# Performance work log

Measured on AMD Instinct MI355X. Metric: run time of the kernel, lower is better.

## Reference

```python
import jax, jax.numpy as jnp
import numpy as np

DIM = 384
H_RES, W_RES = 56, 56
HEADS = 12
WS = 7          # window size
SS = 3          # shift size
N = WS * WS     # tokens per window
NW = (H_RES // WS) * (W_RES // WS)
EPS = 1e-5


def _rel_pos_index(ws):
    coords = np.stack(np.meshgrid(np.arange(ws), np.arange(ws), indexing='ij'))  # [2,ws,ws]
    cf = coords.reshape(2, -1)                      # [2, N]
    rc = (cf[:, :, None] - cf[:, None, :]).transpose(1, 2, 0)  # [N,N,2]
    rc[..., 0] += ws - 1
    rc[..., 1] += ws - 1
    rc[..., 0] *= 2 * ws - 1
    return rc.sum(-1)                               # [N,N] int


def _attn_mask(h, w, ws, ss):
    img = np.zeros((h, w))
    cnt = 0
    slices = (slice(0, -ws), slice(-ws, -ss), slice(-ss, None))
    for hs in slices:
        for wsl in slices:
            img[hs, wsl] = cnt
            cnt += 1
    mw = img.reshape(h // ws, ws, w // ws, ws).transpose(0, 2, 1, 3).reshape(-1, ws * ws)  # [nW,N]
    d = mw[:, None, :] - mw[:, :, None]
    return np.where(d != 0, -100.0, 0.0).astype(np.float32)  # [nW,N,N]


RPI = jnp.asarray(_rel_pos_index(WS).reshape(-1))          # [N*N]
ATTN_MASK = jnp.asarray(_attn_mask(H_RES, W_RES, WS, SS))  # [nW,N,N]


def _layernorm(x, g, b):
    mu = jnp.mean(x, axis=-1, keepdims=True)
    var = jnp.mean(jnp.square(x - mu), axis=-1, keepdims=True)
    return (x - mu) * jax.lax.rsqrt(var + EPS) * g + b


def setup_inputs() -> dict:
    key = jax.random.key(0)
    ks = jax.random.split(key, 8)
    s = 0.02
    return {
        'x': jax.random.normal(ks[0], (32, 1 + H_RES * W_RES, DIM), jnp.float32),
        'norm1_g': jnp.ones((DIM,), jnp.float32),
        'norm1_b': jnp.zeros((DIM,), jnp.float32),
        'qkv_w': jax.random.normal(ks[1], (DIM, 3 * DIM), jnp.float32) * s,
        'qkv_b': jnp.zeros((3 * DIM,), jnp.float32),
        'rpb_table': jax.random.normal(ks[2], ((2 * WS - 1) ** 2, HEADS), jnp.float32) * s,
        'proj_w': jax.random.normal(ks[3], (DIM, DIM), jnp.float32) * s,
        'proj_b': jnp.zeros((DIM,), jnp.float32),
        'norm2_g': jnp.ones((DIM,), jnp.float32),
        'norm2_b': jnp.zeros((DIM,), jnp.float32),
        'fc1_w': jax.random.normal(ks[4], (DIM, 4 * DIM), jnp.float32) * s,
        'fc1_b': jnp.zeros((4 * DIM,), jnp.float32),
        'fc2_w': jax.random.normal(ks[5], (4 * DIM, DIM), jnp.float32) * s,
        'fc2_b': jnp.zeros((DIM,), jnp.float32),
    }


def reference(x, norm1_g, norm1_b, qkv_w, qkv_b, rpb_table, proj_w, proj_b,
              norm2_g, norm2_b, fc1_w, fc1_b, fc2_w, fc2_b):
    B = x.shape[0]
    C = DIM
    hd = C // HEADS
    scale = hd ** -0.5

    time_token = x[:, :1, :]          # [B,1,C]
    img = x[:, 1:, :]                 # [B,H*W,C]
    shortcut = img

    h = _layernorm(img, norm1_g, norm1_b).reshape(B, H_RES, W_RES, C)
    h = jnp.roll(h, shift=(-SS, -SS), axis=(1, 2))  # cyclic shift

    # window partition -> [B*nW, N, C]
    xw = h.reshape(B, H_RES // WS, WS, W_RES // WS, WS, C)
    xw = xw.transpose(0, 1, 3, 2, 4, 5).reshape(-1, N, C)

    # window attention
    qkv = (xw @ qkv_w + qkv_b).reshape(-1, N, 3, HEADS, hd).transpose(2, 0, 3, 1, 4)
    q, k, v = qkv[0], qkv[1], qkv[2]                 # [B*nW, H, N, hd]
    attn = jnp.einsum('whnd,whmd->whnm', q * scale, k)
    bias = rpb_table[RPI].reshape(N, N, HEADS).transpose(2, 0, 1)  # [H,N,N]
    attn = attn + bias[None]
    attn = attn.reshape(B, NW, HEADS, N, N) + ATTN_MASK[None, :, None]
    attn = jax.nn.softmax(attn.reshape(-1, HEADS, N, N), axis=-1)
    out = jnp.einsum('whnm,whmd->wnhd', attn, v).reshape(-1, N, C)
    out = out @ proj_w + proj_b

    # window reverse -> [B,H,W,C]
    out = out.reshape(B, H_RES // WS, W_RES // WS, WS, WS, C)
    out = out.transpose(0, 1, 3, 2, 4, 5).reshape(B, H_RES, W_RES, C)
    out = jnp.roll(out, shift=(SS, SS), axis=(1, 2)).reshape(B, H_RES * W_RES, C)

    img = shortcut + out
    x = jnp.concatenate([time_token, img], axis=1)   # [B,1+H*W,C]
    x = _layernorm(x, norm2_g, norm2_b)
    hmlp = jax.nn.gelu(x @ fc1_w + fc1_b, approximate=False)
    x = x + (hmlp @ fc2_w + fc2_b)
    return x
```

## Files before the change

### kernel.cpp

```cpp
#include <hip/hip_runtime.h>
#include <hip/hip_bf16.h>

#define DIM 384
#define HEADS 12
#define NTOK 49
#define TOKENS 3137
#define M_ATTN 100352
#define M_FULL 100384
#define M_PAD  100480
#define SCALEQ 0.17677669529663687f

typedef __attribute__((ext_vector_type(8))) short s8v;
typedef __attribute__((ext_vector_type(4))) float f4v;
typedef unsigned short u16;

__device__ __forceinline__ float b2f(int s) {
  union { unsigned u; float f; } c; c.u = ((unsigned)(s & 0xffff)) << 16; return c.f;
}
__device__ __forceinline__ u16 f2b(float f) {
  __hip_bfloat16 h = __float2bfloat16(f);
  return *reinterpret_cast<u16*>(&h);
}
__device__ __forceinline__ void gload16(const void* g, void* l) {
  __builtin_amdgcn_global_load_lds((const __attribute__((address_space(1))) void*)g,
                                   (__attribute__((address_space(3))) void*)l, 16, 0, 0);
}

__global__ void k_convert(const float* __restrict__ qkv_w, const float* __restrict__ qkv_b,
                          const float* __restrict__ proj_w, const float* __restrict__ fc1_w,
                          const float* __restrict__ fc2_w,
                          u16* __restrict__ wt_qkv, float* __restrict__ qkvb_s,
                          u16* __restrict__ wt_proj, u16* __restrict__ wt_fc1,
                          u16* __restrict__ wt_fc2) {
  int i = blockIdx.x * 256 + threadIdx.x;
  if (i < 1152 * 384) { int n = i / 384, k = i % 384;
    float v = qkv_w[(size_t)k * 1152 + n]; if (n < 384) v *= SCALEQ; wt_qkv[i] = f2b(v); }
  if (i < 1152) qkvb_s[i] = qkv_b[i] * (i < 384 ? SCALEQ : 1.0f);
  if (i < 384 * 384) { int n = i / 384, k = i % 384; wt_proj[i] = f2b(proj_w[(size_t)k * 384 + n]); }
  if (i < 1536 * 384) { int n = i / 384, k = i % 384; wt_fc1[i] = f2b(fc1_w[(size_t)k * 1536 + n]); }
  if (i < 384 * 1536) { int n = i / 1536, k = i % 1536; wt_fc2[i] = f2b(fc2_w[(size_t)k * 384 + n]); }
}

__global__ void k_addtab(const float* __restrict__ rpb, float* __restrict__ ADD) {
  int idx = blockIdx.x * 256 + threadIdx.x;
  if (idx >= 4 * HEADS * NTOK * NTOK) return;
  int j = idx % NTOK, t = idx / NTOK;
  int i = t % NTOK; t /= NTOK;
  int h = t % HEADS; int cls = t / HEADS;
  int ii = i / 7, jj = i % 7, ji = j / 7, j2 = j % 7;
  int rpi = (ii - ji + 6) * 13 + (jj - j2 + 6);
  float v = rpb[rpi * HEADS + h];
  int rh = (cls & 2) ? (ii < 4 ? 1 : 2) : 0;
  int rw = (cls & 1) ? (jj < 4 ? 1 : 2) : 0;
  int sh = (cls & 2) ? (ji < 4 ? 1 : 2) : 0;
  int sw = (cls & 1) ? (j2 < 4 ? 1 : 2) : 0;
  if (rh != sh || rw != sw) v -= 100.0f;
  ADD[idx] = v;
}

__global__ void k_ln1(const float* __restrict__ x, const float* __restrict__ g,
                      const float* __restrict__ b, u16* __restrict__ xw, int t0) {
  int wid = threadIdx.x >> 6, lane = threadIdx.x & 63;
  int t = t0 + blockIdx.x * 4 + wid;
  int bi = t / 3136, rem = t % 3136;
  int win = rem / NTOK, n = rem % NTOK;
  int wh = win >> 3, ww = win & 7, ii = n / 7, jj = n % 7;
  int h = (wh * 7 + ii + 3) % 56;
  int w = (ww * 7 + jj + 3) % 56;
  const float* src = x + ((size_t)bi * TOKENS + 1 + h * 56 + w) * DIM;
  float v[6];
  #pragma unroll
  for (int e = 0; e < 6; e++) v[e] = src[lane + e * 64];
  float s = v[0] + v[1] + v[2] + v[3] + v[4] + v[5];
  #pragma unroll
  for (int m = 1; m < 64; m <<= 1) s += __shfl_xor(s, m);
  float mu = s * (1.0f / 384.0f);
  float q = 0.f;
  #pragma unroll
  for (int e = 0; e < 6; e++) { float d = v[e] - mu; q += d * d; }
  #pragma unroll
  for (int m = 1; m < 64; m <<= 1) q += __shfl_xor(q, m);
  float rstd = rsqrtf(q * (1.0f / 384.0f) + 1e-5f);
  u16* dst = xw + (size_t)(t - t0) * DIM;
  #pragma unroll
  for (int e = 0; e < 6; e++) {
    int c = lane + e * 64;
    dst[c] = f2b((v[e] - mu) * rstd * g[c] + b[c]);
  }
}

template<int MODE>
__global__ __launch_bounds__(256) void k_gemm(
    const u16* __restrict__ A, const u16* __restrict__ Bt,
    const float* __restrict__ bias, u16* __restrict__ Cb,
    float* __restrict__ outp, const u16* __restrict__ resid,
    int N, int K, int row_off) {
  __shared__ __align__(16) u16 As[2][128 * 64];
  __shared__ __align__(16) u16 Bs[2][128 * 64];
  int gx = gridDim.x;
  int lid = blockIdx.y * gx + blockIdx.x;
  int nwg = gx * gridDim.y;
  int q = nwg >> 3, r = nwg & 7;
  int xcd = lid & 7, loc = lid >> 3;
  int tile = (xcd < r ? xcd * (q + 1) : r * (q + 1) + (xcd - r) * q) + loc;
  int m0 = (tile / gx) * 128, n0 = (tile % gx) * 128;
  int t = threadIdx.x;
  int lane = t & 63, wave = t >> 6;
  int lo = lane & 15, hi = lane >> 4;
  int wr = (wave >> 1) * 64, wc = (wave & 1) * 64;
  int rl = lane >> 3;
  int sl = (lane & 7) ^ rl;
  const u16* Ag = A + (size_t)(m0 + wave * 32 + rl) * K + sl * 8;
  const u16* Bg = Bt + (size_t)(n0 + wave * 32 + rl) * K + sl * 8;
  f4v acc[4][4];
  #pragma unroll
  for (int m = 0; m < 4; m++)
    #pragma unroll
    for (int n = 0; n < 4; n++) acc[m][n] = (f4v)(0.0f);
  int nt = K >> 6;
#define STAGE(buf, kt) do {                                              \
    u16* al_ = As[buf] + wave * 32 * 64;                                 \
    u16* bl_ = Bs[buf] + wave * 32 * 64;                                 \
    _Pragma("unroll")                                                    \
    for (int g_ = 0; g_ < 4; g_++) {                                     \
      gload16(Ag + (size_t)(g_ * 8) * K + (kt), al_ + g_ * 8 * 64);      \
      gload16(Bg + (size_t)(g_ * 8) * K + (kt), bl_ + g_ * 8 * 64);      \
    } } while (0)
  STAGE(0, 0);
  for (int kt = 0; kt < nt; ++kt) {
    int c = kt & 1;
    if (kt + 1 < nt) {
      STAGE(1 - c, (kt + 1) << 6);
      asm volatile("s_waitcnt vmcnt(8)" ::: "memory");
    } else {
      asm volatile("s_waitcnt vmcnt(0)" ::: "memory");
    }
    __builtin_amdgcn_s_barrier();
    __builtin_amdgcn_sched_barrier(0);
    s8v af[2][4], bfr[2][4];
    #pragma unroll
    for (int kk = 0; kk < 2; kk++) {
      #pragma unroll
      for (int m = 0; m < 4; m++) {
        int row = wr + m * 16 + lo;
        af[kk][m] = *(const s8v*)(As[c] + row * 64 + (((kk * 4 + hi) ^ (row & 7)) * 8));
      }
      #pragma unroll
      for (int n = 0; n < 4; n++) {
        int row = wc + n * 16 + lo;
        bfr[kk][n] = *(const s8v*)(Bs[c] + row * 64 + (((kk * 4 + hi) ^ (row & 7)) * 8));
      }
    }
    asm volatile("s_waitcnt lgkmcnt(0)" ::: "memory");
    __builtin_amdgcn_sched_barrier(0);
    __builtin_amdgcn_s_barrier();
    __builtin_amdgcn_sched_barrier(0);
    __builtin_amdgcn_s_setprio(1);
    #pragma unroll
    for (int kk = 0; kk < 2; kk++)
      #pragma unroll
      for (int m = 0; m < 4; m++)
        #pragma unroll
        for (int n = 0; n < 4; n++)
          acc[m][n] = __builtin_amdgcn_mfma_f32_16x16x32_bf16(af[kk][m], bfr[kk][n], acc[m][n], 0, 0, 0);
    __builtin_amdgcn_s_setprio(0);
  }
#undef STAGE
  #pragma unroll
  for (int m = 0; m < 4; m++) {
    int grow = m0 + wr + m * 16 + hi * 4;
    #pragma unroll
    for (int n = 0; n < 4; n++) {
      int gcol = n0 + wc + n * 16 + lo;
      float bv = bias[gcol];
      #pragma unroll
      for (int r2 = 0; r2 < 4; r2++) {
        float val = acc[m][n][r2] + bv;
        size_t idx = (size_t)(grow + r2) * N + gcol;
        if (MODE == 0) {
          Cb[idx] = f2b(val);
        } else if (MODE == 1) {
          float u = __builtin_fmaf(0.0713548163f * val, val * val, 1.5957691216f * val);
          float gl = val * __builtin_amdgcn_rcpf(1.0f + __expf(-u));
          Cb[idx] = f2b(gl);
        } else {
          int orow = grow + r2 + row_off;
          if (orow < M_FULL) {
            size_t oi = (size_t)orow * DIM + gcol;
            outp[oi] = val + b2f(resid[oi]);
          }
        }
      }
    }
  }
}

__global__ __launch_bounds__(256) void k_attn2(const u16* __restrict__ qkv,
                                               const float* __restrict__ ADD,
                                               u16* __restrict__ ao, int win0) {
  __shared__ u16 PT[4][64][76];
  __shared__ u16 VT[4][32][76];
  int wid = threadIdx.x >> 6, lane = threadIdx.x & 63;
  int lo = lane & 15, hi = lane >> 4;
  int win_l = blockIdx.x * 4 + wid;
  int nw = (win0 + win_l) & 63;
  int wh = nw >> 3, ww = nw & 7;
  int cls = ((wh == 7) ? 2 : 0) + ((ww == 7) ? 1 : 0);
  size_t rowbase = (size_t)win_l * NTOK;
  u16 (*pt)[76] = PT[wid];
  u16 (*vt)[76] = VT[wid];

  int rcl[4];
  #pragma unroll
  for (int ti = 0; ti < 4; ti++) {
    int r = ti * 16 + lo;
    rcl[ti] = r < NTOK ? r : NTOK - 1;
  }
  int jrow = lane < NTOK ? lane : NTOK - 1;

  for (int h = 0; h < HEADS; h++) {
    s8v af[4], bf[4];
    #pragma unroll
    for (int ti = 0; ti < 4; ti++) {
      af[ti] = *(const s8v*)(qkv + (rowbase + rcl[ti]) * 1152 + h * 32 + hi * 8);
      bf[ti] = *(const s8v*)(qkv + (rowbase + rcl[ti]) * 1152 + 384 + h * 32 + hi * 8);
    }
    f4v st[4][4];
    #pragma unroll
    for (int mi = 0; mi < 4; mi++)
      #pragma unroll
      for (int ni = 0; ni < 4; ni++)
        st[mi][ni] = __builtin_amdgcn_mfma_f32_16x16x32_bf16(af[mi], bf[ni], (f4v)(0.0f), 0, 0, 0);

    {
      const u16* vsrc = qkv + (rowbase + jrow) * 1152 + 768 + h * 32;
      #pragma unroll
      for (int d0 = 0; d0 < 32; d0 += 8) {
        s8v v = *(const s8v*)(vsrc + d0);
        #pragma unroll
        for (int e = 0; e < 8; e++) vt[d0 + e][lane] = (u16)v[e];
      }
    }

    const float* addb = ADD + ((size_t)cls * HEADS + h) * (NTOK * NTOK);
    #pragma unroll
    for (int mi = 0; mi < 4; mi++)
      #pragma unroll
      for (int ni = 0; ni < 4; ni++) {
        int jj = ni * 16 + lo;
        #pragma unroll
        for (int r = 0; r < 4; r++) {
          int i = mi * 16 + hi * 4 + r;
          if (jj < NTOK) {
            int ic = i < NTOK ? i : NTOK - 1;
            st[mi][ni][r] += addb[ic * NTOK + jj];
          } else st[mi][ni][r] = -1e30f;
        }
      }

    float invl[4][4];
    #pragma unroll
    for (int mi = 0; mi < 4; mi++)
      #pragma unroll
      for (int r = 0; r < 4; r++) {
        float m = fmaxf(fmaxf(st[mi][0][r], st[mi][1][r]), fmaxf(st[mi][2][r], st[mi][3][r]));
        #pragma unroll
        for (int msk = 1; msk < 16; msk <<= 1) m = fmaxf(m, __shfl_xor(m, msk));
        float s = 0.f;
        #pragma unroll
        for (int ni = 0; ni < 4; ni++) {
          float p = __expf(st[mi][ni][r] - m);
          st[mi][ni][r] = p;
          s += p;
        }
        #pragma unroll
        for (int msk = 1; msk < 16; msk <<= 1) s += __shfl_xor(s, msk);
        invl[mi][r] = 1.0f / s;
      }

    #pragma unroll
    for (int ni = 0; ni < 4; ni++)
      #pragma unroll
      for (int mi = 0; mi < 4; mi++) {
        ushort4 pk;
        pk.x = f2b(st[mi][ni][0]); pk.y = f2b(st[mi][ni][1]);
        pk.z = f2b(st[mi][ni][2]); pk.w = f2b(st[mi][ni][3]);
        *(ushort4*)(&pt[ni * 16 + lo][mi * 16 + hi * 4]) = pk;
      }

    f4v ot[4][2];
    #pragma unroll
    for (int mi = 0; mi < 4; mi++)
      #pragma unroll
      for (int dt = 0; dt < 2; dt++) ot[mi][dt] = (f4v)(0.0f);
    #pragma unroll
    for (int kt = 0; kt < 2; kt++) {
      s8v pa[4], vb[2];
      #pragma unroll
      for (int mi = 0; mi < 4; mi++) {
        s8v p;
        #pragma unroll
        for (int e = 0; e < 8; e++) p[e] = (short)pt[kt * 32 + hi * 8 + e][mi * 16 + lo];
        pa[mi] = p;
      }
      #pragma unroll
      for (int dt = 0; dt < 2; dt++) {
        short4 a = *(const short4*)(&vt[dt * 16 + lo][kt * 32 + hi * 8]);
        short4 b = *(const short4*)(&vt[dt * 16 + lo][kt * 32 + hi * 8 + 4]);
        s8v v; v[0] = a.x; v[1] = a.y; v[2] = a.z; v[3] = a.w;
               v[4] = b.x; v[5] = b.y; v[6] = b.z; v[7] = b.w;
        vb[dt] = v;
      }
      #pragma unroll
      for (int mi = 0; mi < 4; mi++)
        #pragma unroll
        for (int dt = 0; dt < 2; dt++)
          ot[mi][dt] = __builtin_amdgcn_mfma_f32_16x16x32_bf16(pa[mi], vb[dt], ot[mi][dt], 0, 0, 0);
    }

    #pragma unroll
    for (int mi = 0; mi < 4; mi++)
      #pragma unroll
      for (int r = 0; r < 4; r++) {
        int i = mi * 16 + hi * 4 + r;
        if (i < NTOK) {
          u16* op = ao + (rowbase + i) * DIM + h * 32 + lo;
          op[0]  = f2b(ot[mi][0][r] * invl[mi][r]);
          op[16] = f2b(ot[mi][1][r] * invl[mi][r]);
        }
      }
  }
}

__global__ void k_ln2(const float* __restrict__ x, const u16* __restrict__ proj,
                      const float* __restrict__ g, const float* __restrict__ b,
                      u16* __restrict__ x2b) {
  int wid = threadIdx.x >> 6, lane = threadIdx.x & 63;
  int r = blockIdx.x * 4 + wid;
  u16* dst = x2b + (size_t)r * DIM;
  if (r >= M_FULL) {
    u16 z = f2b(0.0f);
    #pragma unroll
    for (int e = 0; e < 6; e++) dst[lane + e * 64] = z;
    return;
  }
  int bi = r / TOKENS, tk = r % TOKENS;
  const float* xs = x + (size_t)r * DIM;
  float v[6];
  if (tk == 0) {
    #pragma unroll
    for (int e = 0; e < 6; e++) v[e] = xs[lane + e * 64];
  } else {
    int p = tk - 1, hh = p / 56, wp = p % 56;
    int a = (hh + 53) % 56, bw = (wp + 53) % 56;
    int wh = a / 7, ii = a % 7, w2 = bw / 7, jj = bw % 7;
    size_t prow = ((size_t)bi * 64 + wh * 8 + w2) * NTOK + ii * 7 + jj;
    const u16* ps = proj + prow * DIM;
    #pragma unroll
    for (int e = 0; e < 6; e++) v[e] = xs[lane + e * 64] + b2f(ps[lane + e * 64]);
  }
  float s = v[0] + v[1] + v[2] + v[3] + v[4] + v[5];
  #pragma unroll
  for (int m = 1; m < 64; m <<= 1) s += __shfl_xor(s, m);
  float mu = s * (1.0f / 384.0f);
  float q = 0.f;
  #pragma unroll
  for (int e = 0; e < 6; e++) { float d = v[e] - mu; q += d * d; }
  #pragma unroll
  for (int m = 1; m < 64; m <<= 1) q += __shfl_xor(q, m);
  float rstd = rsqrtf(q * (1.0f / 384.0f) + 1e-5f);
  #pragma unroll
  for (int e = 0; e < 6; e++) {
    int c = lane + e * 64;
    dst[c] = f2b((v[e] - mu) * rstd * g[c] + b[c]);
  }
}

extern "C" void kernel_launch(void* const* d_in, const int* in_sizes, int n_in,
                              void* d_out, int out_size, void* d_ws, size_t ws_size,
                              hipStream_t stream) {
  const float* x      = (const float*)d_in[0];
  const float* n1g    = (const float*)d_in[1];
  const float* n1b    = (const float*)d_in[2];
  const float* qkv_w  = (const float*)d_in[3];
  const float* qkv_b  = (const float*)d_in[4];
  const float* rpb    = (const float*)d_in[5];
  const float* proj_w = (const float*)d_in[6];
  const float* proj_b = (const float*)d_in[7];
  const float* n2g    = (const float*)d_in[8];
  const float* n2b    = (const float*)d_in[9];
  const float* fc1_w  = (const float*)d_in[10];
  const float* fc1_b  = (const float*)d_in[11];
  const float* fc2_w  = (const float*)d_in[12];
  const float* fc2_b  = (const float*)d_in[13];
  float* outp = (float*)d_out;

  auto al = [](size_t v) { return (v + 255) & ~(size_t)255; };
  const int cand[8][2] = {{1,1},{1,2},{2,2},{2,4},{4,4},{4,8},{8,8},{16,16}};
  int NC1 = 16, NC2 = 16;
  for (int ci = 0; ci < 8; ci++) {
    int c1 = cand[ci][0], c2 = cand[ci][1];
    int cbb = (785 + c2 - 1) / c2;
    size_t tot = al(884736) + al(294912) + al(1179648) + al(1179648) + al(4608)
               + al(460992)
               + al((size_t)(M_ATTN / c1) * 768)
               + al((size_t)(M_ATTN / c1) * 2304)
               + al((size_t)M_ATTN * 768)
               + al((size_t)M_PAD * 768)
               + al((size_t)cbb * 128 * 1536 * 2);
    if (tot <= ws_size) { NC1 = c1; NC2 = c2; break; }
  }
  char* p = (char*)d_ws;
  auto take = [&](size_t bytes) { char* r = p; p += al(bytes); return r; };
  u16* wt_qkv  = (u16*)take(884736);
  u16* wt_proj = (u16*)take(294912);
  u16* wt_fc1  = (u16*)take(1179648);
  u16* wt_fc2  = (u16*)take(1179648);
  float* qkvb_s = (float*)take(4608);
  float* ADDt   = (float*)take(460992);
  int chunkM = M_ATTN / NC1;
  u16* XW   = (u16*)take((size_t)chunkM * 768);
  u16* QKV  = (u16*)take((size_t)chunkM * 2304);
  u16* PROJ = (u16*)take((size_t)M_ATTN * 768);
  u16* X2B  = (u16*)take((size_t)M_PAD * 768);
  int cb = (785 + NC2 - 1) / NC2;
  u16* FC1  = (u16*)take((size_t)cb * 128 * 1536 * 2);
  u16* AO = XW;

  k_convert<<<2304, 256, 0, stream>>>(qkv_w, qkv_b, proj_w, fc1_w, fc2_w,
                                      wt_qkv, qkvb_s, wt_proj, wt_fc1, wt_fc2);
  k_addtab<<<451, 256, 0, stream>>>(rpb, ADDt);
  int chunkWin = chunkM / NTOK;
  for (int c = 0; c < NC1; c++) {
    int t0 = c * chunkM;
    k_ln1<<<chunkM / 4, 256, 0, stream>>>(x, n1g, n1b, XW, t0);
    k_gemm<0><<<dim3(9, chunkM / 128), 256, 0, stream>>>(XW, wt_qkv, qkvb_s, QKV,
                                                         nullptr, nullptr, 1152, 384, 0);
    k_attn2<<<chunkWin / 4, 256, 0, stream>>>(QKV, ADDt, AO, c * chunkWin);
    k_gemm<0><<<dim3(3, chunkM / 128), 256, 0, stream>>>(AO, wt_proj, proj_b,
                                                         PROJ + (size_t)t0 * DIM,
                                                         nullptr, nullptr, 384, 384, 0);
  }
  k_ln2<<<M_PAD / 4, 256, 0, stream>>>(x, PROJ, n2g, n2b, X2B);
  for (int c = 0; c < NC2; c++) {
    int rb0 = c * cb;
    int nb = 785 - rb0; if (nb > cb) nb = cb; if (nb <= 0) break;
    k_gemm<1><<<dim3(12, nb), 256, 0, stream>>>(X2B + (size_t)rb0 * 128 * DIM, wt_fc1,
                                                fc1_b, FC1, nullptr, nullptr, 1536, 384, 0);
    k_gemm<2><<<dim3(3, nb), 256, 0, stream>>>(FC1, wt_fc2, fc2_b, nullptr, outp, X2B,
                                               384, 1536, rb0 * 128);
  }
}
```

Baseline: 1.007 ms.

## Fuse LayerNorm1 into QKV GEMM and LayerNorm2 into projection GEMM

Replaces the separate LN1 kernel plus QKV GEMM with one kernel that normalizes a 64-row tile into LDS and then loops over all 1152 output columns. It also replaces the projection GEMM plus LN2 pass with a kernel whose blocks hold full 384-wide rows, so it can add the residual, reduce the row statistics across waves and write the normalized, un-shifted bf16 rows directly into X2B. This removes the XW and PROJ intermediate round-trips and two launches per chunk. In exchange the GEMM tiles are narrower, the projection kernel has no double buffering and waits synchronously on loads, variance is computed as E[x²]−μ², and chunk candidates are restricted to 4, 8 or 16.

```diff
diff --git a/kernel.cpp b/kernel.cpp
--- a/kernel.cpp
+++ b/kernel.cpp
@@ -24,6 +24,10 @@
 __device__ __forceinline__ void gload16(const void* g, void* l) {
   __builtin_amdgcn_global_load_lds((const __attribute__((address_space(1))) void*)g,
                                    (__attribute__((address_space(3))) void*)l, 16, 0, 0);
+}
+__device__ __forceinline__ float gelu_f(float val) {
+  float u = __builtin_fmaf(0.0713548163f * val, val * val, 1.5957691216f * val);
+  return val * __builtin_amdgcn_rcpf(1.0f + __expf(-u));
 }
 
 __global__ void k_convert(const float* __restrict__ qkv_w, const float* __restrict__ qkv_b,
@@ -58,34 +62,246 @@
   ADD[idx] = v;
 }
 
-__global__ void k_ln1(const float* __restrict__ x, const float* __restrict__ g,
-                      const float* __restrict__ b, u16* __restrict__ xw, int t0) {
+__global__ __launch_bounds__(256, 2) void k_lnqkv(
+    const float* __restrict__ x, const float* __restrict__ g1, const float* __restrict__ b1,
+    const u16* __restrict__ Wq, const float* __restrict__ ba,
+    u16* __restrict__ QKV, int t0) {
+  __shared__ __align__(16) u16 Xs[64 * 384];
+  __shared__ __align__(16) u16 Bsb[2][128 * 64];
+  int tid = threadIdx.x, wid = tid >> 6, lane = tid & 63;
+  int lo = lane & 15, hi = lane >> 4;
+  int m0 = blockIdx.x * 64;
+  int q4 = lane >> 4, l16 = lane & 15;
+  #pragma unroll
+  for (int pass = 0; pass < 4; pass++) {
+    int ml = wid * 16 + pass * 4 + q4;
+    int wr = t0 + m0 + ml;
+    int bi = wr / 3136, rem = wr % 3136;
+    int win = rem / NTOK, n = rem % NTOK;
+    int wh = win >> 3, ww = win & 7, ii = n / 7, jj = n % 7;
+    int h = (wh * 7 + ii + 3) % 56, w = (ww * 7 + jj + 3) % 56;
+    const float4* src = (const float4*)(x + ((size_t)bi * TOKENS + 1 + h * 56 + w) * DIM);
+    float4 v[6];
+    #pragma unroll
+    for (int e = 0; e < 6; e++) v[e] = src[l16 + e * 16];
+    float s = 0.f, ss = 0.f;
+    #pragma unroll
+    for (int e = 0; e < 6; e++) {
+      s += v[e].x + v[e].y + v[e].z + v[e].w;
+      ss += v[e].x * v[e].x + v[e].y * v[e].y + v[e].z * v[e].z + v[e].w * v[e].w;
+    }
+    #pragma unroll
+    for (int msk = 1; msk < 16; msk <<= 1) { s += __shfl_xor(s, msk); ss += __shfl_xor(ss, msk); }
+    float mu = s * (1.0f / 384.0f);
+    float rstd = rsqrtf(ss * (1.0f / 384.0f) - mu * mu + 1e-5f);
+    #pragma unroll
+    for (int e = 0; e < 6; e++) {
+      int c0 = e * 64 + l16 * 4;
+      ushort4 pk;
+      pk.x = f2b((v[e].x - mu) * rstd * g1[c0] + b1[c0]);
+      pk.y = f2b((v[e].y - mu) * rstd * g1[c0 + 1] + b1[c0 + 1]);
+      pk.z = f2b((v[e].z - mu) * rstd * g1[c0 + 2] + b1[c0 + 2]);
+      pk.w = f2b((v[e].w - mu) * rstd * g1[c0 + 3] + b1[c0 + 3]);
+      int slot = c0 >> 3, el = c0 & 7;
+      *(ushort4*)(&Xs[ml * 384 + ((slot ^ (ml & 7)) << 3) + el]) = pk;
+    }
+  }
+  __syncthreads();
+  int rl = lane >> 3, sl = (lane & 7) ^ rl;
+  for (int ch = 0; ch < 9; ch++) {
+    const u16* Bg = Wq + (size_t)(ch * 128 + wid * 32 + rl) * 384 + sl * 8;
+    u16* Bl0 = Bsb[0] + wid * 32 * 64;
+    u16* Bl1 = Bsb[1] + wid * 32 * 64;
+    auto stb = [&](int bf, int ks) {
+      u16* dst = bf ? Bl1 : Bl0;
+      #pragma unroll
+      for (int g_ = 0; g_ < 4; g_++)
+        gload16(Bg + (size_t)(g_ * 8) * 384 + ks * 64, dst + g_ * 8 * 64);
+    };
+    f4v acc[4][2];
+    #pragma unroll
+    for (int mi = 0; mi < 4; mi++)
+      #pragma unroll
+      for (int ni = 0; ni < 2; ni++) acc[mi][ni] = (f4v)(0.0f);
+    stb(0, 0);
+    for (int ks = 0; ks < 6; ks++) {
+      int c = ks & 1;
+      if (ks + 1 < 6) {
+        stb(1 - c, ks + 1);
+        asm volatile("s_waitcnt vmcnt(4)" ::: "memory");
+      } else {
+        asm volatile("s_waitcnt vmcnt(0)" ::: "memory");
+      }
+      __builtin_amdgcn_s_barrier();
+      __builtin_amdgcn_sched_barrier(0);
+      s8v a[2][4], bf_[2][2];
+      const u16* Bcur = Bsb[c];
+      #pragma unroll
+      for (int kk = 0; kk < 2; kk++) {
+        #pragma unroll
+        for (int mi = 0; mi < 4; mi++) {
+          int row = mi * 16 + lo;
+          int s2 = ks * 8 + kk * 4 + hi;
+          a[kk][mi] = *(const s8v*)(Xs + row * 384 + ((s2 ^ (row & 7)) << 3));
+        }
+        #pragma unroll
+        for (int ni = 0; ni < 2; ni++) {
+          int row = wid * 32 + ni * 16 + lo;
+          bf_[kk][ni] = *(const s8v*)(Bcur + row * 64 + (((kk * 4 + hi) ^ (row & 7)) << 3));
+        }
+      }
+      asm volatile("s_waitcnt lgkmcnt(0)" ::: "memory");
+      __builtin_amdgcn_sched_barrier(0);
+      __builtin_amdgcn_s_barrier();
+      __builtin_amdgcn_sched_barrier(0);
+      __builtin_amdgcn_s_setprio(1);
+      #pragma unroll
+      for (int kk = 0; kk < 2; kk++)
+        #pragma unroll
+        for (int mi = 0; mi < 4; mi++)
+          #pragma unroll
+          for (int ni = 0; ni < 2; ni++)
+            acc[mi][ni] = __builtin_amdgcn_mfma_f32_16x16x32_bf16(a[kk][mi], bf_[kk][ni], acc[mi][ni], 0, 0, 0);
+      __builtin_amdgcn_s_setprio(0);
+    }
+    #pragma unroll
+    for (int mi = 0; mi < 4; mi++)
+      #pragma unroll
+      for (int ni = 0; ni < 2; ni++) {
+        int gcol = ch * 128 + wid * 32 + ni * 16 + lo;
+        float bv = ba[gcol];
+        #pragma unroll
+        for (int r = 0; r < 4; r++) {
+          int row = m0 + mi * 16 + hi * 4 + r;
+          QKV[(size_t)row * 1152 + gcol] = f2b(acc[mi][ni][r] + bv);
+        }
+      }
+  }
+}
+
+__global__ __launch_bounds__(256, 3) void k_projln(
+    const u16* __restrict__ AO, const u16* __restrict__ Wp, const float* __restrict__ pb,
+    const float* __restrict__ x, const float* __restrict__ g2, const float* __restrict__ b2,
+    u16* __restrict__ X2B, int t0) {
+  __shared__ __align__(16) u16 Bs[384 * 32];
+  __shared__ float part[4][64][2];
+  int tid = threadIdx.x, wid = tid >> 6, lane = tid & 63;
+  int lo = lane & 15, hi = lane >> 4;
+  int nq2 = wid * 96;
+  int m0 = blockIdx.x * 64;
+  int rl2 = lane >> 2, sl2 = (lane & 3) ^ (rl2 & 3);
+  f4v acc[4][6];
+  #pragma unroll
+  for (int mi = 0; mi < 4; mi++)
+    #pragma unroll
+    for (int ni = 0; ni < 6; ni++) acc[mi][ni] = (f4v)(0.0f);
+  for (int kt = 0; kt < 12; kt++) {
+    s8v a[4];
+    #pragma unroll
+    for (int mi = 0; mi < 4; mi++)
+      a[mi] = *(const s8v*)(AO + (size_t)(m0 + mi * 16 + lo) * 384 + kt * 32 + hi * 8);
+    __syncthreads();
+    #pragma unroll
+    for (int i = 0; i < 6; i++) {
+      int gi = wid * 6 + i;
+      gload16(Wp + (size_t)(gi * 16 + rl2) * 384 + kt * 32 + sl2 * 8, (char*)Bs + gi * 1024);
+    }
+    asm volatile("s_waitcnt vmcnt(0)" ::: "memory");
+    __syncthreads();
+    s8v b[6];
+    #pragma unroll
+    for (int ni = 0; ni < 6; ni++) {
+      int row = nq2 + ni * 16 + lo;
+      b[ni] = *(const s8v*)(Bs + row * 32 + ((hi ^ (row & 3)) << 3));
+    }
+    #pragma unroll
+    for (int mi = 0; mi < 4; mi++)
+      #pragma unroll
+      for (int ni = 0; ni < 6; ni++)
+        acc[mi][ni] = __builtin_amdgcn_mfma_f32_16x16x32_bf16(a[mi], b[ni], acc[mi][ni], 0, 0, 0);
+  }
+  float pbv[6], gv[6], bv[6];
+  #pragma unroll
+  for (int ni = 0; ni < 6; ni++) {
+    int gcol = nq2 + ni * 16 + lo;
+    pbv[ni] = pb[gcol]; gv[ni] = g2[gcol]; bv[ni] = b2[gcol];
+  }
+  #pragma unroll
+  for (int mi = 0; mi < 4; mi++)
+    #pragma unroll
+    for (int r = 0; r < 4; r++) {
+      int wr = t0 + m0 + mi * 16 + hi * 4 + r;
+      int bi = wr / 3136, rem = wr % 3136;
+      int win = rem / NTOK, n = rem % NTOK;
+      int wh = win >> 3, ww = win & 7, ii = n / 7, jj = n % 7;
+      int h = (wh * 7 + ii + 3) % 56, w = (ww * 7 + jj + 3) % 56;
+      int tok = bi * TOKENS + 1 + h * 56 + w;
+      const float* xp = x + (size_t)tok * DIM;
+      float s = 0.f, ss = 0.f;
+      #pragma unroll
+      for (int ni = 0; ni < 6; ni++) {
+        float v = acc[mi][ni][r] + pbv[ni] + xp[nq2 + ni * 16 + lo];
+        acc[mi][ni][r] = v;
+        s += v; ss += v * v;
+      }
+      #pragma unroll
+      for (int msk = 1; msk < 16; msk <<= 1) { s += __shfl_xor(s, msk); ss += __shfl_xor(ss, msk); }
+      part[wid][mi * 16 + hi * 4 + r][0] = s;
+      part[wid][mi * 16 + hi * 4 + r][1] = ss;
+    }
+  __syncthreads();
+  #pragma unroll
+  for (int mi = 0; mi < 4; mi++)
+    #pragma unroll
+    for (int r = 0; r < 4; r++) {
+      int wr = t0 + m0 + mi * 16 + hi * 4 + r;
+      int bi = wr / 3136, rem = wr % 3136;
+      int win = rem / NTOK, n = rem % NTOK;
+      int wh = win >> 3, ww = win & 7, ii = n / 7, jj = n % 7;
+      int h = (wh * 7 + ii + 3) % 56, w = (ww * 7 + jj + 3) % 56;
+      int tok = bi * TOKENS + 1 + h * 56 + w;
+      int rloc = mi * 16 + hi * 4 + r;
+      float S = part[0][rloc][0] + part[1][rloc][0] + part[2][rloc][0] + part[3][rloc][0];
+      float SS = part[0][rloc][1] + part[1][rloc][1] + part[2][rloc][1] + part[3][rloc][1];
+      float mu = S * (1.0f / 384.0f);
+      float rstd = rsqrtf(SS * (1.0f / 384.0f) - mu * mu + 1e-5f);
+      u16* op = X2B + (size_t)tok * DIM;
+      #pragma unroll
+      for (int ni = 0; ni < 6; ni++)
+        op[nq2 + ni * 16 + lo] = f2b((acc[mi][ni][r] - mu) * rstd * gv[ni] + bv[ni]);
+    }
+}
+
+__global__ void k_tt(const float* __restrict__ x, const float* __restrict__ g2,
+                     const float* __restrict__ b2, u16* __restrict__ X2B) {
   int wid = threadIdx.x >> 6, lane = threadIdx.x & 63;
-  int t = t0 + blockIdx.x * 4 + wid;
-  int bi = t / 3136, rem = t % 3136;
-  int win = rem / NTOK, n = rem % NTOK;
-  int wh = win >> 3, ww = win & 7, ii = n / 7, jj = n % 7;
-  int h = (wh * 7 + ii + 3) % 56;
-  int w = (ww * 7 + jj + 3) % 56;
-  const float* src = x + ((size_t)bi * TOKENS + 1 + h * 56 + w) * DIM;
-  float v[6];
-  #pragma unroll
-  for (int e = 0; e < 6; e++) v[e] = src[lane + e * 64];
-  float s = v[0] + v[1] + v[2] + v[3] + v[4] + v[5];
-  #pragma unroll
-  for (int m = 1; m < 64; m <<= 1) s += __shfl_xor(s, m);
-  float mu = s * (1.0f / 384.0f);
-  float q = 0.f;
-  #pragma unroll
-  for (int e = 0; e < 6; e++) { float d = v[e] - mu; q += d * d; }
-  #pragma unroll
-  for (int m = 1; m < 64; m <<= 1) q += __shfl_xor(q, m);
-  float rstd = rsqrtf(q * (1.0f / 384.0f) + 1e-5f);
-  u16* dst = xw + (size_t)(t - t0) * DIM;
-  #pragma unroll
-  for (int e = 0; e < 6; e++) {
-    int c = lane + e * 64;
-    dst[c] = f2b((v[e] - mu) * rstd * g[c] + b[c]);
+  int idx = blockIdx.x * 4 + wid;
+  if (idx >= 128) return;
+  if (idx < 32) {
+    size_t row = (size_t)idx * TOKENS;
+    const float* xs = x + row * DIM;
+    float v[6];
+    #pragma unroll
+    for (int e = 0; e < 6; e++) v[e] = xs[lane + e * 64];
+    float s = 0.f, ss = 0.f;
+    #pragma unroll
+    for (int e = 0; e < 6; e++) { s += v[e]; ss += v[e] * v[e]; }
+    #pragma unroll
+    for (int m = 1; m < 64; m <<= 1) { s += __shfl_xor(s, m); ss += __shfl_xor(ss, m); }
+    float mu = s * (1.0f / 384.0f);
+    float rstd = rsqrtf(ss * (1.0f / 384.0f) - mu * mu + 1e-5f);
+    u16* dst = X2B + row * DIM;
+    #pragma unroll
+    for (int e = 0; e < 6; e++) {
+      int c = lane + e * 64;
+      dst[c] = f2b((v[e] - mu) * rstd * g2[c] + b2[c]);
+    }
+  } else {
+    size_t row = (size_t)M_FULL + (idx - 32);
+    u16* dst = X2B + row * DIM;
+    u16 z = f2b(0.0f);
+    #pragma unroll
+    for (int e = 0; e < 6; e++) dst[lane + e * 64] = z;
   }
 }
 
@@ -177,12 +393,8 @@
       for (int r2 = 0; r2 < 4; r2++) {
         float val = acc[m][n][r2] + bv;
         size_t idx = (size_t)(grow + r2) * N + gcol;
-        if (MODE == 0) {
-          Cb[idx] = f2b(val);
-        } else if (MODE == 1) {
-          float u = __builtin_fmaf(0.0713548163f * val, val * val, 1.5957691216f * val);
-          float gl = val * __builtin_amdgcn_rcpf(1.0f + __expf(-u));
-          Cb[idx] = f2b(gl);
+        if (MODE == 1) {
+          Cb[idx] = f2b(gelu_f(val));
         } else {
           int orow = grow + r2 + row_off;
           if (orow < M_FULL) {
@@ -329,50 +541,6 @@
           op[16] = f2b(ot[mi][1][r] * invl[mi][r]);
         }
       }
-  }
-}
-
-__global__ void k_ln2(const float* __restrict__ x, const u16* __restrict__ proj,
-                      const float* __restrict__ g, const float* __restrict__ b,
-                      u16* __restrict__ x2b) {
-  int wid = threadIdx.x >> 6, lane = threadIdx.x & 63;
-  int r = blockIdx.x * 4 + wid;
-  u16* dst = x2b + (size_t)r * DIM;
-  if (r >= M_FULL) {
-    u16 z = f2b(0.0f);
-    #pragma unroll
-    for (int e = 0; e < 6; e++) dst[lane + e * 64] = z;
-    return;
-  }
-  int bi = r / TOKENS, tk = r % TOKENS;
-  const float* xs = x + (size_t)r * DIM;
-  float v[6];
-  if (tk == 0) {
-    #pragma unroll
-    for (int e = 0; e < 6; e++) v[e] = xs[lane + e * 64];
-  } else {
-    int p = tk - 1, hh = p / 56, wp = p % 56;
-    int a = (hh + 53) % 56, bw = (wp + 53) % 56;
-    int wh = a / 7, ii = a % 7, w2 = bw / 7, jj = bw % 7;
-    size_t prow = ((size_t)bi * 64 + wh * 8 + w2) * NTOK + ii * 7 + jj;
-    const u16* ps = proj + prow * DIM;
-    #pragma unroll
-    for (int e = 0; e < 6; e++) v[e] = xs[lane + e * 64] + b2f(ps[lane + e * 64]);
-  }
-  float s = v[0] + v[1] + v[2] + v[3] + v[4] + v[5];
-  #pragma unroll
-  for (int m = 1; m < 64; m <<= 1) s += __shfl_xor(s, m);
-  float mu = s * (1.0f / 384.0f);
-  float q = 0.f;
-  #pragma unroll
-  for (int e = 0; e < 6; e++) { float d = v[e] - mu; q += d * d; }
-  #pragma unroll
-  for (int m = 1; m < 64; m <<= 1) q += __shfl_xor(q, m);
-  float rstd = rsqrtf(q * (1.0f / 384.0f) + 1e-5f);
-  #pragma unroll
-  for (int e = 0; e < 6; e++) {
-    int c = lane + e * 64;
-    dst[c] = f2b((v[e] - mu) * rstd * g[c] + b[c]);
   }
 }
 
@@ -396,17 +564,14 @@
   float* outp = (float*)d_out;
 
   auto al = [](size_t v) { return (v + 255) & ~(size_t)255; };
-  const int cand[8][2] = {{1,1},{1,2},{2,2},{2,4},{4,4},{4,8},{8,8},{16,16}};
+  size_t fixed = al(884736) + al(294912) + al(1179648) + al(1179648) + al(4608)
+               + al(460992) + al((size_t)M_PAD * 768);
+  const int cands[3][2] = {{4, 4}, {8, 8}, {16, 16}};
   int NC1 = 16, NC2 = 16;
-  for (int ci = 0; ci < 8; ci++) {
-    int c1 = cand[ci][0], c2 = cand[ci][1];
+  for (int ci = 0; ci < 3; ci++) {
+    int c1 = cands[ci][0], c2 = cands[ci][1];
     int cbb = (785 + c2 - 1) / c2;
-    size_t tot = al(884736) + al(294912) + al(1179648) + al(1179648) + al(4608)
-               + al(460992)
-               + al((size_t)(M_ATTN / c1) * 768)
-               + al((size_t)(M_ATTN / c1) * 2304)
-               + al((size_t)M_ATTN * 768)
-               + al((size_t)M_PAD * 768)
+    size_t tot = fixed + al((size_t)(M_ATTN / c1) * 2304) + al((size_t)(M_ATTN / c1) * 768)
                + al((size_t)cbb * 128 * 1536 * 2);
     if (tot <= ws_size) { NC1 = c1; NC2 = c2; break; }
   }
@@ -418,30 +583,24 @@
   u16* wt_fc2  = (u16*)take(1179648);
   float* qkvb_s = (float*)take(4608);
   float* ADDt   = (float*)take(460992);
+  u16* X2B  = (u16*)take((size_t)M_PAD * 768);
   int chunkM = M_ATTN / NC1;
-  u16* XW   = (u16*)take((size_t)chunkM * 768);
   u16* QKV  = (u16*)take((size_t)chunkM * 2304);
-  u16* PROJ = (u16*)take((size_t)M_ATTN * 768);
-  u16* X2B  = (u16*)take((size_t)M_PAD * 768);
+  u16* AO   = (u16*)take((size_t)chunkM * 768);
   int cb = (785 + NC2 - 1) / NC2;
   u16* FC1  = (u16*)take((size_t)cb * 128 * 1536 * 2);
-  u16* AO = XW;
 
   k_convert<<<2304, 256, 0, stream>>>(qkv_w, qkv_b, proj_w, fc1_w, fc2_w,
                                       wt_qkv, qkvb_s, wt_proj, wt_fc1, wt_fc2);
   k_addtab<<<451, 256, 0, stream>>>(rpb, ADDt);
+  k_tt<<<32, 256, 0, stream>>>(x, n2g, n2b, X2B);
   int chunkWin = chunkM / NTOK;
   for (int c = 0; c < NC1; c++) {
     int t0 = c * chunkM;
-    k_ln1<<<chunkM / 4, 256, 0, stream>>>(x, n1g, n1b, XW, t0);
-    k_gemm<0><<<dim3(9, chunkM / 128), 256, 0, stream>>>(XW, wt_qkv, qkvb_s, QKV,
-                                                         nullptr, nullptr, 1152, 384, 0);
+    k_lnqkv<<<chunkM / 64, 256, 0, stream>>>(x, n1g, n1b, wt_qkv, qkvb_s, QKV, t0);
     k_attn2<<<chunkWin / 4, 256, 0, stream>>>(QKV, ADDt, AO, c * chunkWin);
-    k_gemm<0><<<dim3(3, chunkM / 128), 256, 0, stream>>>(AO, wt_proj, proj_b,
-                                                         PROJ + (size_t)t0 * DIM,
-                                                         nullptr, nullptr, 384, 384, 0);
-  }
-  k_ln2<<<M_PAD / 4, 256, 0, stream>>>(x, PROJ, n2g, n2b, X2B);
+    k_projln<<<chunkM / 64, 256, 0, stream>>>(AO, wt_proj, proj_b, x, n2g, n2b, X2B, t0);
+  }
   for (int c = 0; c < NC2; c++) {
     int rb0 = c * cb;
     int nb = 785 - rb0; if (nb > cb) nb = cb; if (nb <= 0) break;
```

Result: slower. 1.384 ms (+37.4%).
